# Kernel optimization log

Measured on AMD Instinct MI355X. Metric: run time of the kernel, lower is better.

The kernel has to match this reference:

```python
import jax, jax.numpy as jnp
import numpy as np

B, SD, SE = 4, 2048, 2048
HID, HID_ = 300, 512
N_HEADS = 8


def setup_inputs() -> dict:
    key = jax.random.key(0)
    ks = jax.random.split(key, 7)
    en = jax.random.normal(ks[0], (B, SE, HID), dtype=jnp.float32)
    de = jax.random.normal(ks[1], (B, SD, HID), dtype=jnp.float32)
    mask = jax.random.randint(ks[2], (1, 1, SD, SE), 0, 2).astype(jnp.bool_)
    WQ = jax.random.normal(ks[3], (HID, HID_), dtype=jnp.float32)
    WK = jax.random.normal(ks[4], (HID, HID_), dtype=jnp.float32)
    WV = jax.random.normal(ks[5], (HID, HID_), dtype=jnp.float32)
    WO = jax.random.normal(ks[6], (HID_, HID), dtype=jnp.float32)
    return {"en": en, "de": de, "mask": mask, "WQ": WQ, "WK": WK, "WV": WV, "WO": WO}


def reference(en, de, mask, WQ, WK, WV, WO):
    # Faithful to the torch module (dropout in eval mode => identity).
    d_k = de.shape[-1]  # NOTE: original scales by sqrt(hidden_dim)=sqrt(300), not head_dim
    b_d, s_d = de.shape[0], de.shape[1]
    b_e, s_e = en.shape[0], en.shape[1]
    # head axis is the LAST axis of the reshape (size 8), exactly as the original view/permute
    q = jnp.transpose((de @ WQ).reshape(b_d, s_d, -1, N_HEADS), (3, 0, 1, 2))  # [8,B,Sd,64]
    k = jnp.transpose((en @ WK).reshape(b_e, s_e, -1, N_HEADS), (3, 0, 2, 1))  # [8,B,64,Se]
    v = jnp.transpose((en @ WV).reshape(b_e, s_e, -1, N_HEADS), (3, 0, 1, 2))  # [8,B,Se,64]
    e = jnp.matmul(q, k) / jnp.sqrt(jnp.asarray(d_k, dtype=q.dtype))           # [8,B,Sd,Se]
    e = jnp.where(mask, jnp.asarray(-1e9, dtype=e.dtype), e)
    alpha = jax.nn.softmax(e, axis=3)
    head3 = jnp.matmul(alpha, v)                                               # [8,B,Sd,64]
    # torch.cat((head3[0],...,head3[7]), 2) == move head axis into feature concat order
    a = jnp.concatenate([head3[h] for h in range(N_HEADS)], axis=2)            # [B,Sd,512]
    return a @ WO                                                              # [B,Sd,300]
```

## Files before the change

kernel.cpp:

```cpp
#include <hip/hip_runtime.h>
#include <hip/hip_bf16.h>
#include <math.h>

#define B_      4
#define SD_     2048
#define SE_     2048
#define HIDIN   300
#define HIDMID  512
#define NH      8
#define DH      64
#define ESZ     ((size_t)4194304)
#define BUFB    24576

typedef __attribute__((ext_vector_type(8)))  short          s16x8;
typedef __attribute__((ext_vector_type(8)))  unsigned short u16x8;
typedef __attribute__((ext_vector_type(4)))  unsigned short u16x4;
typedef __attribute__((ext_vector_type(4)))  float          f32x4;
typedef __attribute__((ext_vector_type(16))) float          f32x16;

#define MFMA16 __builtin_amdgcn_mfma_f32_16x16x32_bf16
#define MFMA32 __builtin_amdgcn_mfma_f32_32x32x16_bf16

#define QSCALE  0.0832940411f
#define NEGL   -1.4426950e9f
#define DEFER_THR 24.0f

__device__ __forceinline__ unsigned short f2bf(float f) {
    unsigned int u = __float_as_uint(f);
    u += 0x7fffu + ((u >> 16) & 1u);
    return (unsigned short)(u >> 16);
}
__device__ __forceinline__ float bf2f(unsigned short s) {
    return __uint_as_float((unsigned int)s << 16);
}
__device__ __forceinline__ void gload16(const void* g, void* l) {
    __builtin_amdgcn_global_load_lds(
        (const __attribute__((address_space(1))) void*)g,
        (__attribute__((address_space(3))) void*)l, 16, 0, 0);
}
__device__ __forceinline__ float fexp2(float x) {
#if __has_builtin(__builtin_amdgcn_exp2f)
    return __builtin_amdgcn_exp2f(x);
#else
    return exp2f(x);
#endif
}

#define OF_QH   ((size_t)0)
#define OF_QL   (ESZ)
#define OF_KH   (2*ESZ)
#define OF_KL   (3*ESZ)
#define OF_VT   (4*ESZ)
#define OF_CA   (5*ESZ)
#define OF_CW   (OF_CA + 10485760)
#define OF_WOT  (OF_CW + 983040)

__global__ __launch_bounds__(256) void bias_kernel(const int* __restrict__ mask,
                                                   unsigned int* __restrict__ BiasT)
{
    const int idx = blockIdx.x * 256 + threadIdx.x;
    const int q = idx >> 5, t64 = idx & 31;
    const int* __restrict__ mrow = mask + (size_t)q * SE_ + t64 * 64;
    const unsigned int NEGB = (unsigned int)f2bf(NEGL);
    int mv[64];
#pragma unroll
    for (int i = 0; i < 16; ++i) {
        const int4 mm = *(const int4*)(mrow + i * 4);
        mv[i*4+0] = mm.x; mv[i*4+1] = mm.y; mv[i*4+2] = mm.z; mv[i*4+3] = mm.w;
    }
    uint4* __restrict__ dst4 = (uint4*)BiasT;
    const size_t cbase = ((size_t)(q >> 5) * 32 + t64) * 4;
#pragma unroll
    for (int hi = 0; hi < 2; ++hi) {
#pragma unroll
        for (int L = 0; L < 4; ++L) {
            unsigned int wd[4];
#pragma unroll
            for (int i = 0; i < 4; ++i) {
                const int w = L * 4 + i;
                const int t0 = (w >> 3) * 32 + 2 * (w & 1) + 8 * ((w & 7) >> 1) + 4 * hi;
                wd[i] = (mv[t0] ? NEGB : 0u) | ((mv[t0 + 1] ? NEGB : 0u) << 16);
            }
            dst4[(cbase + L) * 64 + hi * 32 + (q & 31)] =
                make_uint4(wd[0], wd[1], wd[2], wd[3]);
        }
    }
}

__global__ __launch_bounds__(256) void convA_kernel(
    const float* __restrict__ de, const float* __restrict__ en,
    unsigned short* __restrict__ CA)
{
    const int idx = blockIdx.x * 256 + threadIdx.x;
    const int mat = blockIdx.y;
    const float* __restrict__ A = mat ? en : de;
    unsigned short* __restrict__ H = CA + (size_t)mat * 5242880;
    unsigned short* __restrict__ L = H + 2621440;
    const int row = idx / 10, ch = idx - row * 10;
    float v[32];
    if (ch < 9) {
#pragma unroll
        for (int i = 0; i < 8; ++i) {
            const float4 f = *(const float4*)(A + (size_t)row * 300 + ch * 32 + i * 4);
            v[i*4+0] = f.x; v[i*4+1] = f.y; v[i*4+2] = f.z; v[i*4+3] = f.w;
        }
    } else {
#pragma unroll
        for (int i = 0; i < 32; ++i) {
            const int k = 288 + i;
            v[i] = (k < 300) ? A[(size_t)row * 300 + k] : 0.f;
        }
    }
    const int r128 = row & 127;
    const int xr = (r128 >> 1) & 3;
    const size_t tb = ((size_t)(row >> 7) * 10 + ch) * 4096 + r128 * 32;
#pragma unroll
    for (int sub = 0; sub < 4; ++sub) {
        const int slot = sub ^ xr;
        u16x8 hv, lv;
#pragma unroll
        for (int e = 0; e < 8; ++e) {
            const float f = v[sub * 8 + e];
            const unsigned short h = f2bf(f);
            hv[e] = h; lv[e] = f2bf(f - bf2f(h));
        }
        *(u16x8*)(H + tb + slot * 8) = hv;
        *(u16x8*)(L + tb + slot * 8) = lv;
    }
}

__global__ __launch_bounds__(256) void convW_kernel(
    const float* __restrict__ WQ, const float* __restrict__ WK,
    const float* __restrict__ WV, const float* __restrict__ WO,
    unsigned short* __restrict__ CW, unsigned short* __restrict__ WOT)
{
    const int idx = blockIdx.x * 256 + threadIdx.x;
    if (idx < 122880) {
        const int which = idx / 40960;
        const int rem = idx - which * 40960;
        const int k = rem >> 7;
        const int n0 = (rem & 127) * 4;
        const float* __restrict__ W = which == 0 ? WQ : (which == 1 ? WK : WV);
        unsigned short* __restrict__ H = CW + (size_t)which * 327680;
        unsigned short* __restrict__ L = H + 163840;
        const float sc = (which == 0) ? QSCALE : 1.f;
        float4 w = make_float4(0.f, 0.f, 0.f, 0.f);
        if (k < 300) w = *(const float4*)(W + (size_t)k * 512 + n0);
        const float wv4[4] = {w.x * sc, w.y * sc, w.z * sc, w.w * sc};
        const int ch = k >> 5, kk = k & 31;
#pragma unroll
        for (int j = 0; j < 4; ++j) {
            const int n = n0 + j, ntile = n >> 7, nr = n & 127;
            const size_t o = ((size_t)(ntile * 10 + ch) * 128 + nr) * 32
                           + (((kk >> 3) ^ ((nr >> 1) & 3)) << 3) + (kk & 7);
            const unsigned short h = f2bf(wv4[j]);
            H[o] = h;
            if (which < 2) L[o] = f2bf(wv4[j] - bf2f(h));
        }
    } else {
        const int idx2 = idx - 122880;
        const int k = idx2 / 96, n4 = idx2 - k * 96;
        const int n0 = n4 * 4;
        float4 w = make_float4(0.f, 0.f, 0.f, 0.f);
        if (n0 < 300) w = *(const float4*)(WO + (size_t)k * 300 + n0);
        const float wv4[4] = {w.x, w.y, w.z, w.w};
        const int ch = k >> 5, kk = k & 31;
#pragma unroll
        for (int j = 0; j < 4; ++j) {
            const int n = n0 + j, ntile = n >> 7, nr = n & 127;
            const size_t o = ((size_t)(ntile * 16 + ch) * 128 + nr) * 32
                           + (((kk >> 3) ^ ((nr >> 1) & 3)) << 3) + (kk & 7);
            WOT[o] = f2bf(wv4[j]);
        }
    }
}

__global__ __launch_bounds__(256) void proj_qk_kernel(
    const unsigned short* __restrict__ CA, const unsigned short* __restrict__ CW,
    unsigned short* __restrict__ Qh, unsigned short* __restrict__ Ql,
    unsigned short* __restrict__ KhT, unsigned short* __restrict__ KlT)
{
    const int lin = blockIdx.x;
    const int which = lin >> 8;
    const int t = lin & 255;
    const int stile = (t & 7) | ((t >> 5) << 3);
    const int jtile = (t >> 3) & 3;
    const int tid = threadIdx.x, wv = tid >> 6, lane = tid & 63;
    const int li = lane & 15, g = lane >> 4;
    const int wr = wv >> 1, wc = wv & 1;

    __shared__ __align__(16) char LBp[65536];

    const unsigned short* __restrict__ pAh =
        CA + (size_t)which * 5242880 + (size_t)stile * 40960 + tid * 8;
    const unsigned short* __restrict__ pAl = pAh + 2621440;
    const unsigned short* __restrict__ pWh =
        CW + (size_t)which * 327680 + (size_t)jtile * 40960 + tid * 8;
    const unsigned short* __restrict__ pWl = pWh + 163840;

#define STAGEP(ch, bofs) {                                                    \
        char* db = LBp + (bofs) + wv * 1024;                                  \
        const size_t co = (size_t)(ch) * 4096;                                \
        gload16(pAh + co,        db);                                         \
        gload16(pAh + co + 2048, db + 4096);                                  \
        gload16(pAl + co,        db + 8192);                                  \
        gload16(pAl + co + 2048, db + 12288);                                 \
        gload16(pWh + co,        db + 16384);                                 \
        gload16(pWh + co + 2048, db + 20480);                                 \
        gload16(pWl + co,        db + 24576);                                 \
        gload16(pWl + co + 2048, db + 28672);                                 \
    }

    int offA[4], offW[4];
#pragma unroll
    for (int ssub = 0; ssub < 4; ++ssub) {
        const int r = wr * 64 + ssub * 16 + li;
        offA[ssub] = r * 64 + ((g ^ ((r >> 1) & 3)) << 4);
    }
#pragma unroll
    for (int jsub = 0; jsub < 4; ++jsub) {
        const int n = wc * 64 + jsub * 16 + li;
        offW[jsub] = n * 64 + ((g ^ ((n >> 1) & 3)) << 4);
    }

    f32x4 acc[4][4];
#pragma unroll
    for (int i = 0; i < 4; ++i)
#pragma unroll
        for (int j = 0; j < 4; ++j) acc[i][j] = (f32x4){0.f, 0.f, 0.f, 0.f};

    STAGEP(0, 0)
    __syncthreads();

#pragma unroll 1
    for (int ch = 0; ch < 10; ++ch) {
        const int bofs = (ch & 1) * 32768;
        if (ch < 9) STAGEP(ch + 1, bofs ^ 32768)
        const char* bp = LBp + bofs;
        s16x8 ah[4], al[4], wh[4], wl[4];
#pragma unroll
        for (int ssub = 0; ssub < 4; ++ssub) {
            ah[ssub] = *(const s16x8*)(bp + offA[ssub]);
            al[ssub] = *(const s16x8*)(bp + 8192 + offA[ssub]);
        }
#pragma unroll
        for (int jsub = 0; jsub < 4; ++jsub) {
            wh[jsub] = *(const s16x8*)(bp + 16384 + offW[jsub]);
            wl[jsub] = *(const s16x8*)(bp + 24576 + offW[jsub]);
        }
        __builtin_amdgcn_s_setprio(1);
#pragma unroll
        for (int ssub = 0; ssub < 4; ++ssub)
#pragma unroll
            for (int jsub = 0; jsub < 4; ++jsub) {
                acc[ssub][jsub] = MFMA16(ah[ssub], wh[jsub], acc[ssub][jsub], 0, 0, 0);
                acc[ssub][jsub] = MFMA16(ah[ssub], wl[jsub], acc[ssub][jsub], 0, 0, 0);
                acc[ssub][jsub] = MFMA16(al[ssub], wh[jsub], acc[ssub][jsub], 0, 0, 0);
            }
        __builtin_amdgcn_s_setprio(0);
        __syncthreads();
    }
#undef STAGEP

    const int jgbase = jtile * 128 + wc * 64 + li;
    const int sbase0 = stile * 128 + wr * 64 + 4 * g;
#pragma unroll
    for (int jsub = 0; jsub < 4; ++jsub) {
        const int jgg = jgbase + jsub * 16;
        const int d = jgg >> 3, hh = jgg & 7;
#pragma unroll
        for (int ssub = 0; ssub < 4; ++ssub) {
            const f32x4 v = acc[ssub][jsub];
            const int sg0 = sbase0 + ssub * 16;
            const int bbv = sg0 >> 11;
            const int bhn = bbv * 8 + hh;
            const int sl0 = sg0 & 2047;
            if (which == 0) {
                const size_t o = ((size_t)bhn * 2048 + sl0) * 64 + d;
#pragma unroll
                for (int r = 0; r < 4; ++r) {
                    const float val = v[r];
                    const unsigned short hi = f2bf(val);
                    Qh[o + r * 64] = hi;
                    Ql[o + r * 64] = f2bf(val - bf2f(hi));
                }
            } else {
                const int tile = sl0 >> 6, tt0 = sl0 & 63;
                const size_t tb = ((size_t)(bhn * 32 + tile)) << 12;
#pragma unroll
                for (int r = 0; r < 4; ++r) {
                    const int tt = tt0 + r;
                    const size_t o = tb + tt * 64 + (((d >> 3) ^ (tt & 7)) << 3) + (d & 7);
                    const float val = v[r];
                    const unsigned short hi = f2bf(val);
                    KhT[o] = hi;
                    KlT[o] = f2bf(val - bf2f(hi));
                }
            }
        }
    }
}

__global__ __launch_bounds__(256) void proj_v_kernel(
    const unsigned short* __restrict__ CA, const unsigned short* __restrict__ CW,
    unsigned short* __restrict__ VtT)
{
    const int t = blockIdx.x;
    const int stile = (t & 7) | ((t >> 5) << 3);
    const int jtile = (t >> 3) & 3;
    const int tid = threadIdx.x, wv = tid >> 6, lane = tid & 63;
    const int li = lane & 15, g = lane >> 4;
    const int wr = wv >> 1, wc = wv & 1;

    __shared__ __align__(16) char LBv[32768];

    const unsigned short* __restrict__ pAh =
        CA + (size_t)1 * 5242880 + (size_t)stile * 40960 + tid * 8;
    const unsigned short* __restrict__ pWh =
        CW + (size_t)2 * 327680 + (size_t)jtile * 40960 + tid * 8;

#define STAGEV(ch, bofs) {                                                    \
        char* db = LBv + (bofs) + wv * 1024;                                  \
        const size_t co = (size_t)(ch) * 4096;                                \
        gload16(pAh + co,        db);                                         \
        gload16(pAh + co + 2048, db + 4096);                                  \
        gload16(pWh + co,        db + 8192);                                  \
        gload16(pWh + co + 2048, db + 12288);                                 \
    }

    int offA[4], offW[4];
#pragma unroll
    for (int ssub = 0; ssub < 4; ++ssub) {
        const int r = wr * 64 + ssub * 16 + li;
        offA[ssub] = r * 64 + ((g ^ ((r >> 1) & 3)) << 4);
    }
#pragma unroll
    for (int jsub = 0; jsub < 4; ++jsub) {
        const int n = wc * 64 + jsub * 16 + li;
        offW[jsub] = 8192 + n * 64 + ((g ^ ((n >> 1) & 3)) << 4);
    }

    f32x4 acc[4][4];
#pragma unroll
    for (int i = 0; i < 4; ++i)
#pragma unroll
        for (int j = 0; j < 4; ++j) acc[i][j] = (f32x4){0.f, 0.f, 0.f, 0.f};

    STAGEV(0, 0)
    __syncthreads();

#pragma unroll 1
    for (int ch = 0; ch < 10; ++ch) {
        const int bofs = (ch & 1) * 16384;
        if (ch < 9) STAGEV(ch + 1, bofs ^ 16384)
        const char* bp = LBv + bofs;
        s16x8 ah[4], wh[4];
#pragma unroll
        for (int ssub = 0; ssub < 4; ++ssub)
            ah[ssub] = *(const s16x8*)(bp + offA[ssub]);
#pragma unroll
        for (int jsub = 0; jsub < 4; ++jsub)
            wh[jsub] = *(const s16x8*)(bp + offW[jsub]);
        __builtin_amdgcn_s_setprio(1);
#pragma unroll
        for (int ssub = 0; ssub < 4; ++ssub)
#pragma unroll
            for (int jsub = 0; jsub < 4; ++jsub)
                acc[ssub][jsub] = MFMA16(ah[ssub], wh[jsub], acc[ssub][jsub], 0, 0, 0);
        __builtin_amdgcn_s_setprio(0);
        __syncthreads();
    }
#undef STAGEV

    const int jgbase = jtile * 128 + wc * 64 + li;
    const int sbase0 = stile * 128 + wr * 64 + 4 * g;
#pragma unroll
    for (int jsub = 0; jsub < 4; ++jsub) {
        const int jgg = jgbase + jsub * 16;
        const int d = jgg >> 3, hh = jgg & 7;
#pragma unroll
        for (int ssub = 0; ssub < 4; ++ssub) {
            const f32x4 v = acc[ssub][jsub];
            const int sg0 = sbase0 + ssub * 16;
            const int bbv = sg0 >> 11;
            const int bhn = bbv * 8 + hh;
            const int sl0 = sg0 & 2047;
            const int tile = sl0 >> 6, tin0 = sl0 & 63;
            const size_t tb = ((size_t)(bhn * 32 + tile)) << 12;
            const int s_pre = ((tin0 >> 4) << 1) | ((tin0 >> 2) & 1);
            const int j0 = ((tin0 >> 3) & 1) * 4;
            const size_t o = tb + (size_t)d * 64 + ((s_pre ^ (d & 7)) << 3) + j0;
            u16x4 pk;
#pragma unroll
            for (int r = 0; r < 4; ++r) pk[r] = f2bf(v[r]);
            *(u16x4*)(VtT + o) = pk;
        }
    }
}

__global__ __launch_bounds__(256, 2) void attn32_kernel(
    const unsigned short* __restrict__ Qh, const unsigned short* __restrict__ Ql,
    const unsigned short* __restrict__ KhT, const unsigned short* __restrict__ KlT,
    const unsigned short* __restrict__ VtT, const unsigned int* __restrict__ BiasT,
    unsigned short* __restrict__ AOb)
{
    const int lin = blockIdx.x + 16 * blockIdx.y;
    const int qt = (lin >> 3) & 15;
    const int bh = (lin & 7) + ((lin >> 7) << 3);
    const int bb = bh >> 3, hh = bh & 7;
    const int tid = threadIdx.x;
    const int wv = tid >> 6, lane = tid & 63;
    const int hi = lane >> 5, l31 = lane & 31, l7 = lane & 7;
    const int q = qt * 128 + wv * 32 + l31;

    __shared__ __align__(16) char LB[3 * BUFB];

    const size_t qoff = ((size_t)bh * SD_ + q) * DH + hi * 8;
    s16x8 qh[4], ql[4];
#pragma unroll
    for (int c = 0; c < 4; ++c) {
        qh[c] = *(const s16x8*)(Qh + qoff + c * 16);
        ql[c] = *(const s16x8*)(Ql + qoff + c * 16);
    }

    const unsigned short* __restrict__ sKh = KhT + ((size_t)bh << 17) + tid * 8;
    const unsigned short* __restrict__ sKl = KlT + ((size_t)bh << 17) + tid * 8;
    const unsigned short* __restrict__ sVt = VtT + ((size_t)bh << 17) + tid * 8;

    int koff[4];
#pragma unroll
    for (int c = 0; c < 4; ++c)
        koff[c] = l31 * 128 + (((2 * c + hi) ^ l7) << 4);

    const int qg = q >> 5;
    const size_t blane4 = (size_t)hi * 32 + l31;
    const uint4* __restrict__ Bias4 = (const uint4*)BiasT;

#define BIASLOAD(T, R0, R1, R2, R3) {                                         \
        const size_t b4 = (((size_t)qg * 32 + (T)) * 4) * 64 + blane4;        \
        R0 = Bias4[b4];        R1 = Bias4[b4 + 64];                           \
        R2 = Bias4[b4 + 128];  R3 = Bias4[b4 + 192];                          \
    }
#define STAGE(tile, boff)                                                     \
    {                                                                         \
        char* db = LB + (boff) + wv * 1024;                                   \
        const size_t toff = (size_t)(tile) << 12;                             \
        gload16(sKh + toff,        db);                                       \
        gload16(sKh + toff + 2048, db + 4096);                                \
        gload16(sKl + toff,        db + 8192);                                \
        gload16(sKl + toff + 2048, db + 12288);                               \
        gload16(sVt + toff,        db + 16384);                               \
        gload16(sVt + toff + 2048, db + 20480);                               \
    }

    float m = -INFINITY, lacc = 0.f;
    f32x16 O0, O1;
#pragma unroll
    for (int i = 0; i < 16; ++i) { O0[i] = 0.f; O1[i] = 0.f; }

    uint4 cB0, cB1, cB2, cB3, nB0, nB1, nB2, nB3;

#define UNPKW(W, S, r)                                                        \
        S[r]     = __uint_as_float((W) << 16);                                \
        S[r + 1] = __uint_as_float((W) & 0xFFFF0000u);

#define ITER(IT, C0_, C1_, C2_, C3_, N0_, N1_, N2_, N3_)                      \
    {                                                                         \
        BIASLOAD(((IT) + 1) & 31, N0_, N1_, N2_, N3_)                         \
        STAGE(((IT) + 2) & 31, cs)                                            \
        f32x16 sA, sB;                                                        \
        UNPKW(C0_.x, sA, 0)  UNPKW(C0_.y, sA, 2)                              \
        UNPKW(C0_.z, sA, 4)  UNPKW(C0_.w, sA, 6)                              \
        UNPKW(C1_.x, sA, 8)  UNPKW(C1_.y, sA, 10)                             \
        UNPKW(C1_.z, sA, 12) UNPKW(C1_.w, sA, 14)                             \
        UNPKW(C2_.x, sB, 0)  UNPKW(C2_.y, sB, 2)                              \
        UNPKW(C2_.z, sB, 4)  UNPKW(C2_.w, sB, 6)                              \
        UNPKW(C3_.x, sB, 8)  UNPKW(C3_.y, sB, 10)                             \
        UNPKW(C3_.z, sB, 12) UNPKW(C3_.w, sB, 14)                             \
        __builtin_amdgcn_s_setprio(1);                                        \
        _Pragma("unroll")                                                     \
        for (int c = 0; c < 4; ++c) {                                         \
            const s16x8 kh0 = *(const s16x8*)(LB + cc + koff[c]);             \
            const s16x8 kh1 = *(const s16x8*)(LB + cc + 4096 + koff[c]);      \
            const s16x8 kl0 = *(const s16x8*)(LB + cc + 8192 + koff[c]);      \
            const s16x8 kl1 = *(const s16x8*)(LB + cc + 12288 + koff[c]);     \
            sA = MFMA32(kh0, qh[c], sA, 0, 0, 0);                             \
            sA = MFMA32(kh0, ql[c], sA, 0, 0, 0);                             \
            sA = MFMA32(kl0, qh[c], sA, 0, 0, 0);                             \
            sB = MFMA32(kh1, qh[c], sB, 0, 0, 0);                             \
            sB = MFMA32(kh1, ql[c], sB, 0, 0, 0);                             \
            sB = MFMA32(kl1, qh[c], sB, 0, 0, 0);                             \
        }                                                                     \
        __builtin_amdgcn_s_setprio(0);                                        \
        float tv[32];                                                         \
        _Pragma("unroll")                                                     \
        for (int i = 0; i < 16; ++i) { tv[i] = sA[i]; tv[16 + i] = sB[i]; }   \
        _Pragma("unroll")                                                     \
        for (int st = 16; st > 0; st >>= 1)                                   \
            _Pragma("unroll")                                                 \
            for (int i = 0; i < st; ++i) tv[i] = fmaxf(tv[i], tv[i + st]);    \
        const float tmax = tv[0];                                             \
        if (!__all(tmax <= m + DEFER_THR)) {                                  \
            float r = fmaxf(tmax, __shfl_xor(tmax, 32));                      \
            const float mn  = fmaxf(m, r);                                    \
            const float scl = fexp2(m - mn);                                  \
            m = mn;                                                           \
            _Pragma("unroll")                                                 \
            for (int i = 0; i < 16; ++i) { O0[i] *= scl; O1[i] *= scl; }      \
            lacc *= scl;                                                      \
        }                                                                     \
        _Pragma("unroll")                                                     \
        for (int i = 0; i < 16; ++i) {                                        \
            sA[i] = fexp2(sA[i] - m);                                         \
            sB[i] = fexp2(sB[i] - m);                                         \
        }                                                                     \
        float sv[32];                                                         \
        _Pragma("unroll")                                                     \
        for (int i = 0; i < 16; ++i) { sv[i] = sA[i]; sv[16 + i] = sB[i]; }   \
        _Pragma("unroll")                                                     \
        for (int st = 16; st > 0; st >>= 1)                                   \
            _Pragma("unroll")                                                 \
            for (int i = 0; i < st; ++i) sv[i] += sv[i + st];                 \
        lacc += sv[0];                                                        \
        union { s16x8 v; unsigned int w[4]; } P0, P1, P2, P3;                 \
        asm("v_cvt_pk_bf16_f32 %0, %1, %2" : "=v"(P0.w[0]) : "v"(sA[0]),  "v"(sA[1]));  \
        asm("v_cvt_pk_bf16_f32 %0, %1, %2" : "=v"(P0.w[1]) : "v"(sA[2]),  "v"(sA[3]));  \
        asm("v_cvt_pk_bf16_f32 %0, %1, %2" : "=v"(P0.w[2]) : "v"(sA[4]),  "v"(sA[5]));  \
        asm("v_cvt_pk_bf16_f32 %0, %1, %2" : "=v"(P0.w[3]) : "v"(sA[6]),  "v"(sA[7]));  \
        asm("v_cvt_pk_bf16_f32 %0, %1, %2" : "=v"(P1.w[0]) : "v"(sA[8]),  "v"(sA[9]));  \
        asm("v_cvt_pk_bf16_f32 %0, %1, %2" : "=v"(P1.w[1]) : "v"(sA[10]), "v"(sA[11])); \
        asm("v_cvt_pk_bf16_f32 %0, %1, %2" : "=v"(P1.w[2]) : "v"(sA[12]), "v"(sA[13])); \
        asm("v_cvt_pk_bf16_f32 %0, %1, %2" : "=v"(P1.w[3]) : "v"(sA[14]), "v"(sA[15])); \
        asm("v_cvt_pk_bf16_f32 %0, %1, %2" : "=v"(P2.w[0]) : "v"(sB[0]),  "v"(sB[1]));  \
        asm("v_cvt_pk_bf16_f32 %0, %1, %2" : "=v"(P2.w[1]) : "v"(sB[2]),  "v"(sB[3]));  \
        asm("v_cvt_pk_bf16_f32 %0, %1, %2" : "=v"(P2.w[2]) : "v"(sB[4]),  "v"(sB[5]));  \
        asm("v_cvt_pk_bf16_f32 %0, %1, %2" : "=v"(P2.w[3]) : "v"(sB[6]),  "v"(sB[7]));  \
        asm("v_cvt_pk_bf16_f32 %0, %1, %2" : "=v"(P3.w[0]) : "v"(sB[8]),  "v"(sB[9]));  \
        asm("v_cvt_pk_bf16_f32 %0, %1, %2" : "=v"(P3.w[1]) : "v"(sB[10]), "v"(sB[11])); \
        asm("v_cvt_pk_bf16_f32 %0, %1, %2" : "=v"(P3.w[2]) : "v"(sB[12]), "v"(sB[13])); \
        asm("v_cvt_pk_bf16_f32 %0, %1, %2" : "=v"(P3.w[3]) : "v"(sB[14]), "v"(sB[15])); \
        __builtin_amdgcn_s_setprio(1);                                        \
        {                                                                     \
            const s16x8 v0 = *(const s16x8*)(LB + cc + 16384 + koff[0]);      \
            const s16x8 v1 = *(const s16x8*)(LB + cc + 16384 + koff[1]);      \
            const s16x8 v2 = *(const s16x8*)(LB + cc + 16384 + koff[2]);      \
            const s16x8 v3 = *(const s16x8*)(LB + cc + 16384 + koff[3]);      \
            O0 = MFMA32(v0, P0.v, O0, 0, 0, 0);                               \
            O0 = MFMA32(v1, P1.v, O0, 0, 0, 0);                               \
            O0 = MFMA32(v2, P2.v, O0, 0, 0, 0);                               \
            O0 = MFMA32(v3, P3.v, O0, 0, 0, 0);                               \
            const s16x8 w0 = *(const s16x8*)(LB + cc + 20480 + koff[0]);      \
            const s16x8 w1 = *(const s16x8*)(LB + cc + 20480 + koff[1]);      \
            const s16x8 w2 = *(const s16x8*)(LB + cc + 20480 + koff[2]);      \
            const s16x8 w3 = *(const s16x8*)(LB + cc + 20480 + koff[3]);      \
            O1 = MFMA32(w0, P0.v, O1, 0, 0, 0);                               \
            O1 = MFMA32(w1, P1.v, O1, 0, 0, 0);                               \
            O1 = MFMA32(w2, P2.v, O1, 0, 0, 0);                               \
            O1 = MFMA32(w3, P3.v, O1, 0, 0, 0);                               \
        }                                                                     \
        __builtin_amdgcn_s_setprio(0);                                        \
        asm volatile("s_waitcnt vmcnt(6)" ::: "memory");                      \
        __builtin_amdgcn_s_barrier();                                         \
        __builtin_amdgcn_sched_barrier(0);                                    \
        cc += BUFB; if (cc == 3 * BUFB) cc = 0;                               \
        cs += BUFB; if (cs == 3 * BUFB) cs = 0;                               \
    }

    int cc = 0, cs = 2 * BUFB;

    BIASLOAD(0, cB0, cB1, cB2, cB3)
    STAGE(0, 0)
    STAGE(1, BUFB)
    asm volatile("s_waitcnt vmcnt(6)" ::: "memory");
    __builtin_amdgcn_s_barrier();
    __builtin_amdgcn_sched_barrier(0);

#pragma unroll 1
    for (int it = 0; it < 32; it += 2) {
        ITER(it,     cB0, cB1, cB2, cB3, nB0, nB1, nB2, nB3)
        ITER(it + 1, nB0, nB1, nB2, nB3, cB0, cB1, cB2, cB3)
    }

    lacc += __shfl_xor(lacc, 32);
    const float rl = 1.f / lacc;
    const int row = bb * 2048 + q;
    const int r128 = row & 127;
    const int xr = (r128 >> 1) & 3;
    unsigned short* __restrict__ ab = AOb + ((size_t)(row >> 7)) * 65536
                                    + r128 * 32 + 4 * hi;
#pragma unroll
    for (int dt = 0; dt < 2; ++dt) {
        const int ch = hh * 2 + dt;
#pragma unroll
        for (int rg = 0; rg < 4; ++rg) {
            u16x4 pk;
#pragma unroll
            for (int c = 0; c < 4; ++c)
                pk[c] = f2bf((dt ? O1[4 * rg + c] : O0[4 * rg + c]) * rl);
            *(u16x4*)(ab + (size_t)ch * 4096 + ((rg ^ xr) << 3)) = pk;
        }
    }
#undef STAGE
#undef BIASLOAD
#undef UNPKW
#undef ITER
}

__global__ __launch_bounds__(256) void epi_mfma_kernel(
    const unsigned short* __restrict__ AOb, const unsigned short* __restrict__ WOT,
    float* __restrict__ out)
{
    const int stile = blockIdx.x, jtile = blockIdx.y;
    const int tid = threadIdx.x, wv = tid >> 6, lane = tid & 63;
    const int li = lane & 15, g = lane >> 4;

    __shared__ __align__(16) char LBe[24576];

    const unsigned short* __restrict__ pA =
        AOb + (size_t)(stile >> 1) * 65536 + (stile & 1) * 2048 + tid * 8;
    const unsigned short* __restrict__ pW = WOT + (size_t)jtile * 65536 + tid * 8;

#define STAGEE(ch, bofs) {                                                    \
        char* dbA = LBe + (bofs) + wv * 1024;                                 \
        const size_t co = (size_t)(ch) * 4096;                                \
        gload16(pA + co,        dbA);                                         \
        gload16(pW + co,        dbA + 4096);                                  \
        gload16(pW + co + 2048, dbA + 8192);                                  \
    }

    int offA[4], offW[2];
#pragma unroll
    for (int ssub = 0; ssub < 4; ++ssub) {
        const int r = ssub * 16 + li;
        offA[ssub] = r * 64 + ((g ^ ((r >> 1) & 3)) << 4);
    }
#pragma unroll
    for (int jsub = 0; jsub < 2; ++jsub) {
        const int n = wv * 32 + jsub * 16 + li;
        offW[jsub] = 4096 + n * 64 + ((g ^ ((n >> 1) & 3)) << 4);
    }

    f32x4 acc[4][2];
#pragma unroll
    for (int i = 0; i < 4; ++i)
#pragma unroll
        for (int j = 0; j < 2; ++j) acc[i][j] = (f32x4){0.f, 0.f, 0.f, 0.f};

    STAGEE(0, 0)
    __syncthreads();

#pragma unroll 1
    for (int ch = 0; ch < 16; ++ch) {
        const int bofs = (ch & 1) * 12288;
        if (ch < 15) STAGEE(ch + 1, bofs ^ 12288)
        const char* bp = LBe + bofs;
        s16x8 ah[4], wh[2];
#pragma unroll
        for (int ssub = 0; ssub < 4; ++ssub)
            ah[ssub] = *(const s16x8*)(bp + offA[ssub]);
#pragma unroll
        for (int jsub = 0; jsub < 2; ++jsub)
            wh[jsub] = *(const s16x8*)(bp + offW[jsub]);
        __builtin_amdgcn_s_setprio(1);
#pragma unroll
        for (int ssub = 0; ssub < 4; ++ssub)
#pragma unroll
            for (int jsub = 0; jsub < 2; ++jsub)
                acc[ssub][jsub] = MFMA16(ah[ssub], wh[jsub], acc[ssub][jsub], 0, 0, 0);
        __builtin_amdgcn_s_setprio(0);
        __syncthreads();
    }
#undef STAGEE

    const int nbase = jtile * 128 + wv * 32 + li;
    const int rbase = stile * 64 + 4 * g;
#pragma unroll
    for (int jsub = 0; jsub < 2; ++jsub) {
        const int o = nbase + jsub * 16;
        if (o < HIDIN) {
#pragma unroll
            for (int ssub = 0; ssub < 4; ++ssub) {
                const f32x4 v = acc[ssub][jsub];
                const int r0 = rbase + ssub * 16;
#pragma unroll
                for (int r = 0; r < 4; ++r)
                    out[(size_t)(r0 + r) * HIDIN + o] = v[r];
            }
        }
    }
}

extern "C" void kernel_launch(void* const* d_in, const int* in_sizes, int n_in,
                              void* d_out, int out_size, void* d_ws, size_t ws_size,
                              hipStream_t stream)
{
    const float* en  = (const float*)d_in[0];
    const float* de  = (const float*)d_in[1];
    const int*   mask = (const int*)d_in[2];
    const float* WQ  = (const float*)d_in[3];
    const float* WK  = (const float*)d_in[4];
    const float* WV  = (const float*)d_in[5];
    const float* WO  = (const float*)d_in[6];
    float* out = (float*)d_out;

    unsigned short* ws2 = (unsigned short*)d_ws;
    unsigned short* Qh  = ws2 + OF_QH;
    unsigned short* Ql  = ws2 + OF_QL;
    unsigned short* KhT = ws2 + OF_KH;
    unsigned short* KlT = ws2 + OF_KL;
    unsigned short* VtT = ws2 + OF_VT;
    unsigned short* CA  = ws2 + OF_CA;
    unsigned short* CW  = ws2 + OF_CW;
    unsigned short* WOT = ws2 + OF_WOT;
    unsigned short* AOb = CA;
    unsigned int*  BiasT = (unsigned int*)(CA + 4194304);

    convA_kernel<<<dim3(320, 2), 256, 0, stream>>>(de, en, CA);
    convW_kernel<<<dim3(672), 256, 0, stream>>>(WQ, WK, WV, WO, CW, WOT);
    proj_qk_kernel<<<dim3(512), 256, 0, stream>>>(CA, CW, Qh, Ql, KhT, KlT);
    proj_v_kernel<<<dim3(256), 256, 0, stream>>>(CA, CW, VtT);
    bias_kernel<<<dim3(256), 256, 0, stream>>>(mask, BiasT);
    attn32_kernel<<<dim3(16, 32), 256, 0, stream>>>(Qh, Ql, KhT, KlT, VtT,
                                                    BiasT, AOb);
    epi_mfma_kernel<<<dim3(128, 3), 256, 0, stream>>>(AOb, WOT, out);
}
```

Baseline: 179.6 us.

## Halve attention KV tile to 32 keys and raise occupancy to four blocks

Shrinks the per-iteration key tile from 64 to 32 keys, halving the shared-memory stage buffers and the score and P registers, and doubles the loop count. The V transpose layout is changed to split each 64-key tile into two 32-key halves with a new swizzle, and V reads use new offsets. Launch bounds are raised to allow four blocks per CU, aiming to hide latency through more resident waves. In exchange there are twice as many barriers and softmax rescale steps, and each barrier covers less MFMA work.

```diff
diff --git a/kernel.cpp b/kernel.cpp
--- a/kernel.cpp
+++ b/kernel.cpp
@@ -10,7 +10,7 @@
 #define NH      8
 #define DH      64
 #define ESZ     ((size_t)4194304)
-#define BUFB    24576
+#define BUFB    12288
 
 typedef __attribute__((ext_vector_type(8)))  short          s16x8;
 typedef __attribute__((ext_vector_type(8)))  unsigned short u16x8;
@@ -387,9 +387,11 @@
             const int sl0 = sg0 & 2047;
             const int tile = sl0 >> 6, tin0 = sl0 & 63;
             const size_t tb = ((size_t)(bhn * 32 + tile)) << 12;
-            const int s_pre = ((tin0 >> 4) << 1) | ((tin0 >> 2) & 1);
-            const int j0 = ((tin0 >> 3) & 1) * 4;
-            const size_t o = tb + (size_t)d * 64 + ((s_pre ^ (d & 7)) << 3) + j0;
+            const int half = (tin0 >> 5) & 1;
+            const int s2 = 2 * ((tin0 >> 4) & 1) + ((tin0 >> 2) & 1);
+            const int j0 = 4 * ((tin0 >> 3) & 1);
+            const size_t o = tb + half * 2048 + (size_t)d * 32
+                           + ((s2 ^ ((d >> 1) & 3)) << 3) + j0;
             u16x4 pk;
 #pragma unroll
             for (int r = 0; r < 4; ++r) pk[r] = f2bf(v[r]);
@@ -398,7 +400,7 @@
     }
 }
 
-__global__ __launch_bounds__(256, 2) void attn32_kernel(
+__global__ __launch_bounds__(256, 4) void attn32_kernel(
     const unsigned short* __restrict__ Qh, const unsigned short* __restrict__ Ql,
     const unsigned short* __restrict__ KhT, const unsigned short* __restrict__ KlT,
     const unsigned short* __restrict__ VtT, const unsigned int* __restrict__ BiasT,
@@ -432,25 +434,30 @@
     for (int c = 0; c < 4; ++c)
         koff[c] = l31 * 128 + (((2 * c + hi) ^ l7) << 4);
 
+    const int swzv = (l31 >> 1) & 3;
+    int voff[2][2];
+#pragma unroll
+    for (int oh = 0; oh < 2; ++oh)
+#pragma unroll
+        for (int tc = 0; tc < 2; ++tc)
+            voff[oh][tc] = (oh * 32 + l31) * 64 + (((2 * tc + hi) ^ swzv) << 4);
+
     const int qg = q >> 5;
     const size_t blane4 = (size_t)hi * 32 + l31;
     const uint4* __restrict__ Bias4 = (const uint4*)BiasT;
 
-#define BIASLOAD(T, R0, R1, R2, R3) {                                         \
-        const size_t b4 = (((size_t)qg * 32 + (T)) * 4) * 64 + blane4;        \
-        R0 = Bias4[b4];        R1 = Bias4[b4 + 64];                           \
-        R2 = Bias4[b4 + 128];  R3 = Bias4[b4 + 192];                          \
-    }
-#define STAGE(tile, boff)                                                     \
+#define BIASLOAD(T32, R0, R1) {                                               \
+        const size_t b4 = (((size_t)qg * 32 + ((T32) >> 1)) * 4               \
+                           + ((T32) & 1) * 2) * 64 + blane4;                  \
+        R0 = Bias4[b4]; R1 = Bias4[b4 + 64];                                  \
+    }
+#define STAGE(t32, boff)                                                      \
     {                                                                         \
         char* db = LB + (boff) + wv * 1024;                                   \
-        const size_t toff = (size_t)(tile) << 12;                             \
-        gload16(sKh + toff,        db);                                       \
-        gload16(sKh + toff + 2048, db + 4096);                                \
-        gload16(sKl + toff,        db + 8192);                                \
-        gload16(sKl + toff + 2048, db + 12288);                               \
-        gload16(sVt + toff,        db + 16384);                               \
-        gload16(sVt + toff + 2048, db + 20480);                               \
+        const size_t toff = (size_t)(t32) << 11;                              \
+        gload16(sKh + toff, db);                                              \
+        gload16(sKl + toff, db + 4096);                                       \
+        gload16(sVt + toff, db + 8192);                                       \
     }
 
     float m = -INFINITY, lacc = 0.f;
@@ -458,45 +465,36 @@
 #pragma unroll
     for (int i = 0; i < 16; ++i) { O0[i] = 0.f; O1[i] = 0.f; }
 
-    uint4 cB0, cB1, cB2, cB3, nB0, nB1, nB2, nB3;
+    uint4 cB0, cB1, nB0, nB1;
 
 #define UNPKW(W, S, r)                                                        \
         S[r]     = __uint_as_float((W) << 16);                                \
         S[r + 1] = __uint_as_float((W) & 0xFFFF0000u);
 
-#define ITER(IT, C0_, C1_, C2_, C3_, N0_, N1_, N2_, N3_)                      \
+#define ITER(IT, C0_, C1_, N0_, N1_)                                          \
     {                                                                         \
-        BIASLOAD(((IT) + 1) & 31, N0_, N1_, N2_, N3_)                         \
-        STAGE(((IT) + 2) & 31, cs)                                            \
-        f32x16 sA, sB;                                                        \
+        BIASLOAD(((IT) + 1) & 63, N0_, N1_)                                   \
+        STAGE(((IT) + 2) & 63, cs)                                            \
+        f32x16 sA;                                                            \
         UNPKW(C0_.x, sA, 0)  UNPKW(C0_.y, sA, 2)                              \
         UNPKW(C0_.z, sA, 4)  UNPKW(C0_.w, sA, 6)                              \
         UNPKW(C1_.x, sA, 8)  UNPKW(C1_.y, sA, 10)                             \
         UNPKW(C1_.z, sA, 12) UNPKW(C1_.w, sA, 14)                             \
-        UNPKW(C2_.x, sB, 0)  UNPKW(C2_.y, sB, 2)                              \
-        UNPKW(C2_.z, sB, 4)  UNPKW(C2_.w, sB, 6)                              \
-        UNPKW(C3_.x, sB, 8)  UNPKW(C3_.y, sB, 10)                             \
-        UNPKW(C3_.z, sB, 12) UNPKW(C3_.w, sB, 14)                             \
         __builtin_amdgcn_s_setprio(1);                                        \
         _Pragma("unroll")                                                     \
         for (int c = 0; c < 4; ++c) {                                         \
-            const s16x8 kh0 = *(const s16x8*)(LB + cc + koff[c]);             \
-            const s16x8 kh1 = *(const s16x8*)(LB + cc + 4096 + koff[c]);      \
-            const s16x8 kl0 = *(const s16x8*)(LB + cc + 8192 + koff[c]);      \
-            const s16x8 kl1 = *(const s16x8*)(LB + cc + 12288 + koff[c]);     \
-            sA = MFMA32(kh0, qh[c], sA, 0, 0, 0);                             \
-            sA = MFMA32(kh0, ql[c], sA, 0, 0, 0);                             \
-            sA = MFMA32(kl0, qh[c], sA, 0, 0, 0);                             \
-            sB = MFMA32(kh1, qh[c], sB, 0, 0, 0);                             \
-            sB = MFMA32(kh1, ql[c], sB, 0, 0, 0);                             \
-            sB = MFMA32(kl1, qh[c], sB, 0, 0, 0);                             \
+            const s16x8 kh = *(const s16x8*)(LB + cc + koff[c]);              \
+            const s16x8 kl = *(const s16x8*)(LB + cc + 4096 + koff[c]);       \
+            sA = MFMA32(kh, qh[c], sA, 0, 0, 0);                              \
+            sA = MFMA32(kh, ql[c], sA, 0, 0, 0);                              \
+            sA = MFMA32(kl, qh[c], sA, 0, 0, 0);                              \
         }                                                                     \
         __builtin_amdgcn_s_setprio(0);                                        \
-        float tv[32];                                                         \
+        float tv[16];                                                         \
         _Pragma("unroll")                                                     \
-        for (int i = 0; i < 16; ++i) { tv[i] = sA[i]; tv[16 + i] = sB[i]; }   \
+        for (int i = 0; i < 16; ++i) tv[i] = sA[i];                           \
         _Pragma("unroll")                                                     \
-        for (int st = 16; st > 0; st >>= 1)                                   \
+        for (int st = 8; st > 0; st >>= 1)                                    \
             _Pragma("unroll")                                                 \
             for (int i = 0; i < st; ++i) tv[i] = fmaxf(tv[i], tv[i + st]);    \
         const float tmax = tv[0];                                             \
@@ -510,19 +508,16 @@
             lacc *= scl;                                                      \
         }                                                                     \
         _Pragma("unroll")                                                     \
-        for (int i = 0; i < 16; ++i) {                                        \
-            sA[i] = fexp2(sA[i] - m);                                         \
-            sB[i] = fexp2(sB[i] - m);                                         \
-        }                                                                     \
-        float sv[32];                                                         \
+        for (int i = 0; i < 16; ++i) sA[i] = fexp2(sA[i] - m);                \
+        float sv[16];                                                         \
         _Pragma("unroll")                                                     \
-        for (int i = 0; i < 16; ++i) { sv[i] = sA[i]; sv[16 + i] = sB[i]; }   \
+        for (int i = 0; i < 16; ++i) sv[i] = sA[i];                           \
         _Pragma("unroll")                                                     \
-        for (int st = 16; st > 0; st >>= 1)                                   \
+        for (int st = 8; st > 0; st >>= 1)                                    \
             _Pragma("unroll")                                                 \
             for (int i = 0; i < st; ++i) sv[i] += sv[i + st];                 \
         lacc += sv[0];                                                        \
-        union { s16x8 v; unsigned int w[4]; } P0, P1, P2, P3;                 \
+        union { s16x8 v; unsigned int w[4]; } P0, P1;                         \
         asm("v_cvt_pk_bf16_f32 %0, %1, %2" : "=v"(P0.w[0]) : "v"(sA[0]),  "v"(sA[1]));  \
         asm("v_cvt_pk_bf16_f32 %0, %1, %2" : "=v"(P0.w[1]) : "v"(sA[2]),  "v"(sA[3]));  \
         asm("v_cvt_pk_bf16_f32 %0, %1, %2" : "=v"(P0.w[2]) : "v"(sA[4]),  "v"(sA[5]));  \
@@ -531,35 +526,19 @@
         asm("v_cvt_pk_bf16_f32 %0, %1, %2" : "=v"(P1.w[1]) : "v"(sA[10]), "v"(sA[11])); \
         asm("v_cvt_pk_bf16_f32 %0, %1, %2" : "=v"(P1.w[2]) : "v"(sA[12]), "v"(sA[13])); \
         asm("v_cvt_pk_bf16_f32 %0, %1, %2" : "=v"(P1.w[3]) : "v"(sA[14]), "v"(sA[15])); \
-        asm("v_cvt_pk_bf16_f32 %0, %1, %2" : "=v"(P2.w[0]) : "v"(sB[0]),  "v"(sB[1]));  \
-        asm("v_cvt_pk_bf16_f32 %0, %1, %2" : "=v"(P2.w[1]) : "v"(sB[2]),  "v"(sB[3]));  \
-        asm("v_cvt_pk_bf16_f32 %0, %1, %2" : "=v"(P2.w[2]) : "v"(sB[4]),  "v"(sB[5]));  \
-        asm("v_cvt_pk_bf16_f32 %0, %1, %2" : "=v"(P2.w[3]) : "v"(sB[6]),  "v"(sB[7]));  \
-        asm("v_cvt_pk_bf16_f32 %0, %1, %2" : "=v"(P3.w[0]) : "v"(sB[8]),  "v"(sB[9]));  \
-        asm("v_cvt_pk_bf16_f32 %0, %1, %2" : "=v"(P3.w[1]) : "v"(sB[10]), "v"(sB[11])); \
-        asm("v_cvt_pk_bf16_f32 %0, %1, %2" : "=v"(P3.w[2]) : "v"(sB[12]), "v"(sB[13])); \
-        asm("v_cvt_pk_bf16_f32 %0, %1, %2" : "=v"(P3.w[3]) : "v"(sB[14]), "v"(sB[15])); \
         __builtin_amdgcn_s_setprio(1);                                        \
         {                                                                     \
-            const s16x8 v0 = *(const s16x8*)(LB + cc + 16384 + koff[0]);      \
-            const s16x8 v1 = *(const s16x8*)(LB + cc + 16384 + koff[1]);      \
-            const s16x8 v2 = *(const s16x8*)(LB + cc + 16384 + koff[2]);      \
-            const s16x8 v3 = *(const s16x8*)(LB + cc + 16384 + koff[3]);      \
-            O0 = MFMA32(v0, P0.v, O0, 0, 0, 0);                               \
-            O0 = MFMA32(v1, P1.v, O0, 0, 0, 0);                               \
-            O0 = MFMA32(v2, P2.v, O0, 0, 0, 0);                               \
-            O0 = MFMA32(v3, P3.v, O0, 0, 0, 0);                               \
-            const s16x8 w0 = *(const s16x8*)(LB + cc + 20480 + koff[0]);      \
-            const s16x8 w1 = *(const s16x8*)(LB + cc + 20480 + koff[1]);      \
-            const s16x8 w2 = *(const s16x8*)(LB + cc + 20480 + koff[2]);      \
-            const s16x8 w3 = *(const s16x8*)(LB + cc + 20480 + koff[3]);      \
-            O1 = MFMA32(w0, P0.v, O1, 0, 0, 0);                               \
-            O1 = MFMA32(w1, P1.v, O1, 0, 0, 0);                               \
-            O1 = MFMA32(w2, P2.v, O1, 0, 0, 0);                               \
-            O1 = MFMA32(w3, P3.v, O1, 0, 0, 0);                               \
+            const s16x8 v00 = *(const s16x8*)(LB + cc + 8192 + voff[0][0]);   \
+            const s16x8 v01 = *(const s16x8*)(LB + cc + 8192 + voff[0][1]);   \
+            const s16x8 v10 = *(const s16x8*)(LB + cc + 8192 + voff[1][0]);   \
+            const s16x8 v11 = *(const s16x8*)(LB + cc + 8192 + voff[1][1]);   \
+            O0 = MFMA32(v00, P0.v, O0, 0, 0, 0);                              \
+            O0 = MFMA32(v01, P1.v, O0, 0, 0, 0);                              \
+            O1 = MFMA32(v10, P0.v, O1, 0, 0, 0);                              \
+            O1 = MFMA32(v11, P1.v, O1, 0, 0, 0);                              \
         }                                                                     \
         __builtin_amdgcn_s_setprio(0);                                        \
-        asm volatile("s_waitcnt vmcnt(6)" ::: "memory");                      \
+        asm volatile("s_waitcnt vmcnt(3)" ::: "memory");                      \
         __builtin_amdgcn_s_barrier();                                         \
         __builtin_amdgcn_sched_barrier(0);                                    \
         cc += BUFB; if (cc == 3 * BUFB) cc = 0;                               \
@@ -568,17 +547,17 @@
 
     int cc = 0, cs = 2 * BUFB;
 
-    BIASLOAD(0, cB0, cB1, cB2, cB3)
+    BIASLOAD(0, cB0, cB1)
     STAGE(0, 0)
     STAGE(1, BUFB)
-    asm volatile("s_waitcnt vmcnt(6)" ::: "memory");
+    asm volatile("s_waitcnt vmcnt(3)" ::: "memory");
     __builtin_amdgcn_s_barrier();
     __builtin_amdgcn_sched_barrier(0);
 
 #pragma unroll 1
-    for (int it = 0; it < 32; it += 2) {
-        ITER(it,     cB0, cB1, cB2, cB3, nB0, nB1, nB2, nB3)
-        ITER(it + 1, nB0, nB1, nB2, nB3, cB0, cB1, cB2, cB3)
+    for (int it = 0; it < 64; it += 2) {
+        ITER(it,     cB0, cB1, nB0, nB1)
+        ITER(it + 1, nB0, nB1, cB0, cB1)
     }
 
     lacc += __shfl_xor(lacc, 32);
```

New measurement: 198.2 us. 1.1x slower.
